# Kernel tuning notes

Hardware: AMD Instinct MI355X
Metric: run time of the kernel (lower is better)

The kernel has to match this reference:

```python
import jax, jax.numpy as jnp
import numpy as np

SIZE = 11
SIGMA = 1.5
ALPHA = 0.7
K1 = 0.01
K2 = 0.03
DATA_RANGE = 1.0
DN = ('NCDHW', 'OIDHW', 'NCDHW')


def _gauss1d():
    ax = jnp.arange(SIZE, dtype=jnp.float32) - SIZE // 2
    k = jnp.exp(-(ax ** 2) / (2.0 * SIGMA * SIGMA))
    return k / k.sum()


def _blur3d(x, k1):
    # Separable depthwise 3D gaussian blur with zero ('constant') padding.
    # Mathematically identical to the dense 11x11x11 outer-product conv3d
    # in the torch source (zero padding commutes with separable passes).
    ch = x.shape[1]
    pad = SIZE // 2
    for kshape in ((SIZE, 1, 1), (1, SIZE, 1), (1, 1, SIZE)):
        w = jnp.broadcast_to(k1.reshape(1, 1, *kshape), (ch, 1) + kshape)
        pads = [(pad, pad) if s == SIZE else (0, 0) for s in kshape]
        x = jax.lax.conv_general_dilated(
            x, w, window_strides=(1, 1, 1), padding=pads,
            dimension_numbers=DN, feature_group_count=ch)
    return x


def setup_inputs() -> dict:
    key = jax.random.key(0)
    k1, k2 = jax.random.split(key)
    shape = (2, 1, 160, 160, 160)
    pred = jax.random.uniform(k1, shape, dtype=jnp.float32)
    target = jax.random.uniform(k2, shape, dtype=jnp.float32)
    return {"pred": pred, "target": target}


def reference(pred, target):
    k1d = _gauss1d()
    pred32 = pred.astype(jnp.float32)
    target32 = target.astype(jnp.float32)

    # L1
    l1 = jnp.mean(jnp.abs(pred32 - target32))

    # SSIM3D
    mu1 = _blur3d(pred32, k1d)
    mu2 = _blur3d(target32, k1d)
    mu1_sq = mu1 * mu1
    mu2_sq = mu2 * mu2
    mu1_mu2 = mu1 * mu2
    sigma1_sq = _blur3d(pred32 * pred32, k1d) - mu1_sq
    sigma2_sq = _blur3d(target32 * target32, k1d) - mu2_sq
    sigma12 = _blur3d(pred32 * target32, k1d) - mu1_mu2

    C1 = (K1 * DATA_RANGE) ** 2
    C2 = (K2 * DATA_RANGE) ** 2
    ssim_map = ((2.0 * mu1_mu2 + C1) * (2.0 * sigma12 + C2)) / (
        (mu1_sq + mu2_sq + C1) * (sigma1_sq + sigma2_sq + C2) + 1e-12)
    ssim = jnp.mean(ssim_map)

    return ALPHA * l1 + (1.0 - ALPHA) * (1.0 - ssim)
```

## Files before the change

kernel.cpp:

```cpp
#include <hip/hip_runtime.h>

typedef float v2f __attribute__((ext_vector_type(2)));

#define DHW 160
#define PLANE (160*160)
#define VOL (160*160*160)
#define PAD 5
#define KS 11
#define TXW 16
#define TYH 32
#define LZ 32
#define SRX 26
#define SRY 42
#define XA2 18
#define XC  24
#define NSLOT 5
#define STAGE_NP (SRY*SRX)
#define NITER ((LZ + 2*PAD) / 2)
#define NBLOCKS 500
#define CNT_POISON 0xAAAAAAAAu

__device__ __forceinline__ void gauss_w(float w[KS]) {
    float s = 0.f;
#pragma unroll
    for (int i = 0; i < KS; ++i) {
        float d = (float)(i - PAD);
        w[i] = expf(-(d * d) / (2.f * 1.5f * 1.5f));
        s += w[i];
    }
    float inv = 1.f / s;
#pragma unroll
    for (int i = 0; i < KS; ++i) w[i] *= inv;
}

__device__ __forceinline__ float block_reduce(float v, float* sm) {
#pragma unroll
    for (int off = 32; off > 0; off >>= 1)
        v += __shfl_down(v, off);
    int lane = threadIdx.x & 63;
    int wid  = threadIdx.x >> 6;
    if (lane == 0) sm[wid] = v;
    __syncthreads();
    float r = 0.f;
    if (threadIdx.x == 0) r = sm[0] + sm[1] + sm[2] + sm[3];
    return r;
}

__global__ __launch_bounds__(256, 2) void k_fused(
    const float* __restrict__ pred, const float* __restrict__ targ,
    double* __restrict__ accum, unsigned* __restrict__ cnt,
    float* __restrict__ out)
{
    __shared__ __align__(16) v2f   sIn[2][SRY][SRX];
    __shared__ __align__(16) v2f   sXBa[2][SRY][XA2];
    __shared__ __align__(16) v2f   sXBb[2][SRY][XA2];
    __shared__ __align__(16) float sXBc[2][SRY][XC];
    __shared__ float sRed[4];

    float gw[KS]; gauss_w(gw);

    const int tile = blockIdx.x;
    const int xt = tile % 10, yt = tile / 10;
    const int z0 = blockIdx.y * LZ;
    const int b  = blockIdx.z;
    const float* __restrict__ P = pred + (size_t)b * VOL;
    const float* __restrict__ T = targ + (size_t)b * VOL;
    const ptrdiff_t dTP = T - P;

    const int tid = threadIdx.x;
    const int tx  = tid & 15;
    const int ty2 = tid >> 4;
    const int y0  = 2 * ty2;

    const float* sptrP[NSLOT];
    bool sact[NSLOT];
    bool sl1[NSLOT];
#pragma unroll
    for (int i = 0; i < NSLOT; ++i) {
        int idx = tid + 256 * i;
        bool act = idx < STAGE_NP;
        int idc = act ? idx : 0;
        int r   = idc / SRX;
        int c   = idc - r * SRX;
        int gy = yt * TYH + r - PAD;
        int gx = xt * TXW + c - PAD;
        bool inp = (gy >= 0 && gy < DHW && gx >= 0 && gx < DHW);
        sact[i] = act && inp;
        sl1[i]  = act && (r >= PAD && r < PAD + TYH) && (c >= PAD && c < PAD + TXW);
        sptrP[i] = P + (inp ? (gy * DHW + gx) : 0);
    }

    auto stage_fetch = [&](int zz, float vp[NSLOT], float vt[NSLOT]) {
        bool zok = (zz >= 0 && zz < DHW);
        size_t zo = (size_t)(zok ? zz : 0) * PLANE;
#pragma unroll
        for (int i = 0; i < NSLOT; ++i) {
            bool ok = zok && sact[i];
            vp[i] = ok ? sptrP[i][zo] : 0.f;
            vt[i] = ok ? sptrP[i][zo + dTP] : 0.f;
        }
    };
    auto stage_write = [&](int slice, const float vp[NSLOT], const float vt[NSLOT]) {
        v2f* base = &sIn[slice][0][0];
#pragma unroll
        for (int i = 0; i < NSLOT; ++i) {
            int idx = tid + 256 * i;
            if (idx < STAGE_NP) {
                v2f w; w.x = vp[i]; w.y = vt[i];
                base[idx] = w;
            }
        }
    };

    auto xblur_unit = [&](int s, int r4, int cg) {
        const float4* row = (const float4*)&sIn[s][r4][0];
        v2f pt[14];
#pragma unroll
        for (int m = 0; m < 7; ++m) {
            float4 q = row[2 * cg + m];
            v2f lo; lo.x = q.x; lo.y = q.y;
            v2f hi; hi.x = q.z; hi.y = q.w;
            pt[2 * m]     = lo;
            pt[2 * m + 1] = hi;
        }
        v2f mm[14]; float pc[14];
#pragma unroll
        for (int i = 0; i < 14; ++i) {
            mm[i] = pt[i] * pt[i];
            pc[i] = pt[i].x * pt[i].y;
        }
        v2f a01[4], a23[4]; float a4[4];
#pragma unroll
        for (int oo = 0; oo < 4; ++oo) { a01[oo] = 0.f; a23[oo] = 0.f; a4[oo] = 0.f; }
#pragma unroll
        for (int j = 0; j < KS; ++j) {
            float w = gw[j];
#pragma unroll
            for (int oo = 0; oo < 4; ++oo) {
                a01[oo] += pt[oo + j] * w;
                a23[oo] += mm[oo + j] * w;
                a4[oo]  += pc[oo + j] * w;
            }
        }
        float4* wa = (float4*)&sXBa[s][r4][0];
        float4 qa0, qa1;
        qa0.x = a01[0].x; qa0.y = a01[0].y; qa0.z = a01[1].x; qa0.w = a01[1].y;
        qa1.x = a01[2].x; qa1.y = a01[2].y; qa1.z = a01[3].x; qa1.w = a01[3].y;
        wa[2 * cg] = qa0; wa[2 * cg + 1] = qa1;
        float4* wb = (float4*)&sXBb[s][r4][0];
        float4 qb0, qb1;
        qb0.x = a23[0].x; qb0.y = a23[0].y; qb0.z = a23[1].x; qb0.w = a23[1].y;
        qb1.x = a23[2].x; qb1.y = a23[2].y; qb1.z = a23[3].x; qb1.w = a23[3].y;
        wb[2 * cg] = qb0; wb[2 * cg + 1] = qb1;
        float4* wc = (float4*)&sXBc[s][r4][0];
        float4 qc; qc.x = a4[0]; qc.y = a4[1]; qc.z = a4[2]; qc.w = a4[3];
        wc[cg] = qc;
    };

    v2f pend01[2][KS], pend23[2][KS];
    float pend4[2][KS];
#pragma unroll
    for (int o = 0; o < 2; ++o)
#pragma unroll
        for (int j = 0; j < KS; ++j) {
            pend01[o][j] = 0.f; pend23[o][j] = 0.f; pend4[o][j] = 0.f;
        }

    float l1s = 0.f, sss = 0.f;
    const float C1 = 0.01f * 0.01f;
    const float C2 = 0.03f * 0.03f;

    auto yblur_push = [&](int s, bool doEmit) {
        v2f t01[KS + 1], t23[KS + 1]; float t4[KS + 1];
#pragma unroll
        for (int j = 0; j < KS + 1; ++j) {
            t01[j] = sXBa[s][y0 + j][tx];
            t23[j] = sXBb[s][y0 + j][tx];
            t4[j]  = sXBc[s][y0 + j][tx];
        }
        v2f a01[2], a23[2]; float a4[2];
        a01[0] = 0.f; a01[1] = 0.f; a23[0] = 0.f; a23[1] = 0.f; a4[0] = 0.f; a4[1] = 0.f;
#pragma unroll
        for (int j = 0; j < KS; ++j) {
            float w = gw[j];
            a01[0] += t01[j] * w;  a01[1] += t01[j + 1] * w;
            a23[0] += t23[j] * w;  a23[1] += t23[j + 1] * w;
            a4[0]  += t4[j]  * w;  a4[1]  += t4[j + 1]  * w;
        }
#pragma unroll
        for (int o = 0; o < 2; ++o) {
#pragma unroll
            for (int i = 0; i < KS - 1; ++i) {
                float w = gw[10 - i];
                pend01[o][i] = pend01[o][i + 1] + a01[o] * w;
                pend23[o][i] = pend23[o][i + 1] + a23[o] * w;
                pend4[o][i]  = pend4[o][i + 1]  + a4[o]  * w;
            }
            pend01[o][10] = a01[o] * gw[0];
            pend23[o][10] = a23[o] * gw[0];
            pend4[o][10]  = a4[o]  * gw[0];
        }
        if (doEmit) {
#pragma unroll
            for (int o = 0; o < 2; ++o) {
                v2f m = pend01[o][0], e = pend23[o][0];
                float e12 = pend4[o][0];
                float mu11 = m.x * m.x, mu22 = m.y * m.y, mu12 = m.x * m.y;
                float s1 = e.x - mu11, s2 = e.y - mu22, s12 = e12 - mu12;
                float num = (2.f * mu12 + C1) * (2.f * s12 + C2);
                float den = (mu11 + mu22 + C1) * (s1 + s2 + C2) + 1e-12f;
                sss += num * __builtin_amdgcn_rcpf(den);
            }
        }
    };

    {
        float vp[NSLOT], vt[NSLOT];
        stage_fetch(z0 - PAD, vp, vt);
        stage_write(0, vp, vt);
        stage_fetch(z0 - PAD + 1, vp, vt);
        stage_write(1, vp, vt);
    }
    __syncthreads();

    for (int m = 0; m < NITER; ++m) {
        const int jA = 2 * m + 2, jB = 2 * m + 3;
        float pA[NSLOT], tA[NSLOT], pB[NSLOT], tB[NSLOT];
        const bool doStage = (m < NITER - 1);

        if (doStage) {
            stage_fetch(z0 - PAD + jA, pA, tA);
            stage_fetch(z0 - PAD + jB, pB, tB);
            if ((unsigned)(jA - PAD) < (unsigned)LZ) {
#pragma unroll
                for (int i = 0; i < NSLOT; ++i)
                    if (sl1[i]) l1s += fabsf(pA[i] - tA[i]);
            }
            if ((unsigned)(jB - PAD) < (unsigned)LZ) {
#pragma unroll
                for (int i = 0; i < NSLOT; ++i)
                    if (sl1[i]) l1s += fabsf(pB[i] - tB[i]);
            }
        }

        {
            int u = tid;
            int s = u / 168, rem = u - s * 168;
            xblur_unit(s, rem >> 2, rem & 3);
            if (tid < 336 - 256) {
                int rem2 = tid + 256 - 168;
                xblur_unit(1, rem2 >> 2, rem2 & 3);
            }
        }

        __syncthreads();

        if (doStage) {
            stage_write(0, pA, tA);
            stage_write(1, pB, tB);
        }

        const bool em = (m >= 5);
        yblur_push(0, em);
        yblur_push(1, em);

        __syncthreads();
    }

    float r1 = block_reduce(l1s, sRed);
    __syncthreads();
    float r2 = block_reduce(sss, sRed);
    if (tid == 0) {
        atomicAdd(&accum[0], (double)r1);
        atomicAdd(&accum[1], (double)r2);
        __threadfence();
        unsigned prev = atomicAdd(cnt, 1u);
        if (prev == CNT_POISON + (unsigned)NBLOCKS - 1u) {
            const double n = 8192000.0;
            double l1   = atomicAdd(&accum[0], 0.0) / n;
            double ssim = atomicAdd(&accum[1], 0.0) / n;
            out[0] = (float)(0.7 * l1 + 0.3 * (1.0 - ssim));
        }
    }
}

extern "C" void kernel_launch(void* const* d_in, const int* in_sizes, int n_in,
                              void* d_out, int out_size, void* d_ws, size_t ws_size,
                              hipStream_t stream) {
    const float* pred = (const float*)d_in[0];
    const float* targ = (const float*)d_in[1];
    float* out = (float*)d_out;
    double* accum = (double*)d_ws;
    unsigned* cnt = (unsigned*)((char*)d_ws + 64);

    dim3 grid(50, DHW / LZ, 2);
    k_fused<<<grid, 256, 0, stream>>>(pred, targ, accum, cnt, out);
}
```

Baseline: 180.5 us.

## Merge variance channels and shrink tile to 16x16 for higher occupancy

The x-blur now blurs p²+t² as a single channel, since SSIM only needs sigma1²+sigma2². That cuts the blurred channels from five to four and drops the separate pc shared buffer. The y tile shrinks from 32 to 16 rows, so each thread emits one output row instead of two. The grid doubles to 1000 blocks and launch bounds allow 4 blocks per CU, aiming for lower register and LDS pressure and better latency hiding. The cost is more y-halo redundancy: 26 staged rows per 16 outputs instead of 42 per 32, which means more global/L2 reads and x-blur work per output.

Result: slower. 209.2 us (+15.9%).

```diff
diff --git a/kernel.cpp b/kernel.cpp
--- a/kernel.cpp
+++ b/kernel.cpp
@@ -8,16 +8,15 @@
 #define PAD 5
 #define KS 11
 #define TXW 16
-#define TYH 32
+#define TYH 16
 #define LZ 32
 #define SRX 26
-#define SRY 42
+#define SRY 26
 #define XA2 18
-#define XC  24
-#define NSLOT 5
+#define NSLOT 3
 #define STAGE_NP (SRY*SRX)
 #define NITER ((LZ + 2*PAD) / 2)
-#define NBLOCKS 500
+#define NBLOCKS 1000
 #define CNT_POISON 0xAAAAAAAAu
 
 __device__ __forceinline__ void gauss_w(float w[KS]) {
@@ -46,7 +45,7 @@
     return r;
 }
 
-__global__ __launch_bounds__(256, 2) void k_fused(
+__global__ __launch_bounds__(256, 4) void k_fused(
     const float* __restrict__ pred, const float* __restrict__ targ,
     double* __restrict__ accum, unsigned* __restrict__ cnt,
     float* __restrict__ out)
@@ -54,7 +53,6 @@
     __shared__ __align__(16) v2f   sIn[2][SRY][SRX];
     __shared__ __align__(16) v2f   sXBa[2][SRY][XA2];
     __shared__ __align__(16) v2f   sXBb[2][SRY][XA2];
-    __shared__ __align__(16) float sXBc[2][SRY][XC];
     __shared__ float sRed[4];
 
     float gw[KS]; gauss_w(gw);
@@ -69,8 +67,7 @@
 
     const int tid = threadIdx.x;
     const int tx  = tid & 15;
-    const int ty2 = tid >> 4;
-    const int y0  = 2 * ty2;
+    const int ty  = tid >> 4;
 
     const float* sptrP[NSLOT];
     bool sact[NSLOT];
@@ -116,101 +113,83 @@
         const float4* row = (const float4*)&sIn[s][r4][0];
         v2f pt[14];
 #pragma unroll
-        for (int m = 0; m < 7; ++m) {
-            float4 q = row[2 * cg + m];
+        for (int m2 = 0; m2 < 7; ++m2) {
+            float4 q = row[2 * cg + m2];
             v2f lo; lo.x = q.x; lo.y = q.y;
             v2f hi; hi.x = q.z; hi.y = q.w;
-            pt[2 * m]     = lo;
-            pt[2 * m + 1] = hi;
-        }
-        v2f mm[14]; float pc[14];
+            pt[2 * m2]     = lo;
+            pt[2 * m2 + 1] = hi;
+        }
+        v2f sc[14];
 #pragma unroll
         for (int i = 0; i < 14; ++i) {
-            mm[i] = pt[i] * pt[i];
-            pc[i] = pt[i].x * pt[i].y;
-        }
-        v2f a01[4], a23[4]; float a4[4];
-#pragma unroll
-        for (int oo = 0; oo < 4; ++oo) { a01[oo] = 0.f; a23[oo] = 0.f; a4[oo] = 0.f; }
+            v2f q = pt[i] * pt[i];
+            sc[i].x = q.x + q.y;
+            sc[i].y = pt[i].x * pt[i].y;
+        }
+        v2f aA[4], aB[4];
+#pragma unroll
+        for (int oo = 0; oo < 4; ++oo) { aA[oo] = 0.f; aB[oo] = 0.f; }
 #pragma unroll
         for (int j = 0; j < KS; ++j) {
             float w = gw[j];
 #pragma unroll
             for (int oo = 0; oo < 4; ++oo) {
-                a01[oo] += pt[oo + j] * w;
-                a23[oo] += mm[oo + j] * w;
-                a4[oo]  += pc[oo + j] * w;
+                aA[oo] += pt[oo + j] * w;
+                aB[oo] += sc[oo + j] * w;
             }
         }
         float4* wa = (float4*)&sXBa[s][r4][0];
         float4 qa0, qa1;
-        qa0.x = a01[0].x; qa0.y = a01[0].y; qa0.z = a01[1].x; qa0.w = a01[1].y;
-        qa1.x = a01[2].x; qa1.y = a01[2].y; qa1.z = a01[3].x; qa1.w = a01[3].y;
+        qa0.x = aA[0].x; qa0.y = aA[0].y; qa0.z = aA[1].x; qa0.w = aA[1].y;
+        qa1.x = aA[2].x; qa1.y = aA[2].y; qa1.z = aA[3].x; qa1.w = aA[3].y;
         wa[2 * cg] = qa0; wa[2 * cg + 1] = qa1;
         float4* wb = (float4*)&sXBb[s][r4][0];
         float4 qb0, qb1;
-        qb0.x = a23[0].x; qb0.y = a23[0].y; qb0.z = a23[1].x; qb0.w = a23[1].y;
-        qb1.x = a23[2].x; qb1.y = a23[2].y; qb1.z = a23[3].x; qb1.w = a23[3].y;
+        qb0.x = aB[0].x; qb0.y = aB[0].y; qb0.z = aB[1].x; qb0.w = aB[1].y;
+        qb1.x = aB[2].x; qb1.y = aB[2].y; qb1.z = aB[3].x; qb1.w = aB[3].y;
         wb[2 * cg] = qb0; wb[2 * cg + 1] = qb1;
-        float4* wc = (float4*)&sXBc[s][r4][0];
-        float4 qc; qc.x = a4[0]; qc.y = a4[1]; qc.z = a4[2]; qc.w = a4[3];
-        wc[cg] = qc;
-    };
-
-    v2f pend01[2][KS], pend23[2][KS];
-    float pend4[2][KS];
-#pragma unroll
-    for (int o = 0; o < 2; ++o)
-#pragma unroll
-        for (int j = 0; j < KS; ++j) {
-            pend01[o][j] = 0.f; pend23[o][j] = 0.f; pend4[o][j] = 0.f;
-        }
+    };
+
+    v2f pendA[KS], pendB[KS];
+#pragma unroll
+    for (int j = 0; j < KS; ++j) { pendA[j] = 0.f; pendB[j] = 0.f; }
 
     float l1s = 0.f, sss = 0.f;
     const float C1 = 0.01f * 0.01f;
     const float C2 = 0.03f * 0.03f;
 
     auto yblur_push = [&](int s, bool doEmit) {
-        v2f t01[KS + 1], t23[KS + 1]; float t4[KS + 1];
-#pragma unroll
-        for (int j = 0; j < KS + 1; ++j) {
-            t01[j] = sXBa[s][y0 + j][tx];
-            t23[j] = sXBb[s][y0 + j][tx];
-            t4[j]  = sXBc[s][y0 + j][tx];
-        }
-        v2f a01[2], a23[2]; float a4[2];
-        a01[0] = 0.f; a01[1] = 0.f; a23[0] = 0.f; a23[1] = 0.f; a4[0] = 0.f; a4[1] = 0.f;
+        v2f tA[KS], tB[KS];
+#pragma unroll
+        for (int j = 0; j < KS; ++j) {
+            tA[j] = sXBa[s][ty + j][tx];
+            tB[j] = sXBb[s][ty + j][tx];
+        }
+        v2f aA, aB; aA = 0.f; aB = 0.f;
 #pragma unroll
         for (int j = 0; j < KS; ++j) {
             float w = gw[j];
-            a01[0] += t01[j] * w;  a01[1] += t01[j + 1] * w;
-            a23[0] += t23[j] * w;  a23[1] += t23[j + 1] * w;
-            a4[0]  += t4[j]  * w;  a4[1]  += t4[j + 1]  * w;
-        }
-#pragma unroll
-        for (int o = 0; o < 2; ++o) {
-#pragma unroll
-            for (int i = 0; i < KS - 1; ++i) {
-                float w = gw[10 - i];
-                pend01[o][i] = pend01[o][i + 1] + a01[o] * w;
-                pend23[o][i] = pend23[o][i + 1] + a23[o] * w;
-                pend4[o][i]  = pend4[o][i + 1]  + a4[o]  * w;
-            }
-            pend01[o][10] = a01[o] * gw[0];
-            pend23[o][10] = a23[o] * gw[0];
-            pend4[o][10]  = a4[o]  * gw[0];
-        }
+            aA += tA[j] * w;
+            aB += tB[j] * w;
+        }
+#pragma unroll
+        for (int i = 0; i < KS - 1; ++i) {
+            float w = gw[10 - i];
+            pendA[i] = pendA[i + 1] + aA * w;
+            pendB[i] = pendB[i + 1] + aB * w;
+        }
+        pendA[10] = aA * gw[0];
+        pendB[10] = aB * gw[0];
         if (doEmit) {
-#pragma unroll
-            for (int o = 0; o < 2; ++o) {
-                v2f m = pend01[o][0], e = pend23[o][0];
-                float e12 = pend4[o][0];
-                float mu11 = m.x * m.x, mu22 = m.y * m.y, mu12 = m.x * m.y;
-                float s1 = e.x - mu11, s2 = e.y - mu22, s12 = e12 - mu12;
-                float num = (2.f * mu12 + C1) * (2.f * s12 + C2);
-                float den = (mu11 + mu22 + C1) * (s1 + s2 + C2) + 1e-12f;
-                sss += num * __builtin_amdgcn_rcpf(den);
-            }
+            v2f mv = pendA[0], ev = pendB[0];
+            float mu11 = mv.x * mv.x, mu22 = mv.y * mv.y, mu12 = mv.x * mv.y;
+            float musum = mu11 + mu22;
+            float s1s2  = ev.x - musum;
+            float s12   = ev.y - mu12;
+            float num = (2.f * mu12 + C1) * (2.f * s12 + C2);
+            float den = (musum + C1) * (s1s2 + C2) + 1e-12f;
+            sss += num * __builtin_amdgcn_rcpf(den);
         }
     };
 
@@ -225,39 +204,35 @@
 
     for (int m = 0; m < NITER; ++m) {
         const int jA = 2 * m + 2, jB = 2 * m + 3;
-        float pA[NSLOT], tA[NSLOT], pB[NSLOT], tB[NSLOT];
+        float pA[NSLOT], tAv[NSLOT], pB[NSLOT], tBv[NSLOT];
         const bool doStage = (m < NITER - 1);
 
         if (doStage) {
-            stage_fetch(z0 - PAD + jA, pA, tA);
-            stage_fetch(z0 - PAD + jB, pB, tB);
+            stage_fetch(z0 - PAD + jA, pA, tAv);
+            stage_fetch(z0 - PAD + jB, pB, tBv);
             if ((unsigned)(jA - PAD) < (unsigned)LZ) {
 #pragma unroll
                 for (int i = 0; i < NSLOT; ++i)
-                    if (sl1[i]) l1s += fabsf(pA[i] - tA[i]);
+                    if (sl1[i]) l1s += fabsf(pA[i] - tAv[i]);
             }
             if ((unsigned)(jB - PAD) < (unsigned)LZ) {
 #pragma unroll
                 for (int i = 0; i < NSLOT; ++i)
-                    if (sl1[i]) l1s += fabsf(pB[i] - tB[i]);
-            }
-        }
-
-        {
-            int u = tid;
-            int s = u / 168, rem = u - s * 168;
+                    if (sl1[i]) l1s += fabsf(pB[i] - tBv[i]);
+            }
+        }
+
+        if (tid < 208) {
+            int s   = (tid >= 104) ? 1 : 0;
+            int rem = tid - s * 104;
             xblur_unit(s, rem >> 2, rem & 3);
-            if (tid < 336 - 256) {
-                int rem2 = tid + 256 - 168;
-                xblur_unit(1, rem2 >> 2, rem2 & 3);
-            }
         }
 
         __syncthreads();
 
         if (doStage) {
-            stage_write(0, pA, tA);
-            stage_write(1, pB, tB);
+            stage_write(0, pA, tAv);
+            stage_write(1, pB, tBv);
         }
 
         const bool em = (m >= 5);
@@ -293,6 +268,6 @@
     double* accum = (double*)d_ws;
     unsigned* cnt = (unsigned*)((char*)d_ws + 64);
 
-    dim3 grid(50, DHW / LZ, 2);
+    dim3 grid(100, DHW / LZ, 2);
     k_fused<<<grid, 256, 0, stream>>>(pred, targ, accum, cnt, out);
 }
```
